# Performance work log

Measured on AMD Instinct MI355X. Metric: run time of the kernel, lower is better.

## Reference

```python
import jax, jax.numpy as jnp
import numpy as np

B, T, D, H, DFF, E = 4, 1024, 1024, 16, 4096, 8
DH = D // H
EPS = 1e-6


def setup_inputs() -> dict:
    key = jax.random.key(0)
    ks = jax.random.split(key, 16)
    s = 0.02
    return {
        "x": jax.random.normal(ks[0], (B, T, D), jnp.float32),
        "mask": jnp.ones((B, 1, 1, T), jnp.bool_),
        "Wq": jax.random.normal(ks[1], (D, D), jnp.float32) * s,
        "bq": jnp.zeros((D,), jnp.float32),
        "Wk": jax.random.normal(ks[2], (D, D), jnp.float32) * s,
        "bk": jnp.zeros((D,), jnp.float32),
        "Wv": jax.random.normal(ks[3], (D, D), jnp.float32) * s,
        "bv": jnp.zeros((D,), jnp.float32),
        "Wo": jax.random.normal(ks[4], (D, D), jnp.float32) * s,
        "bo": jnp.zeros((D,), jnp.float32),
        "ln1_a": jnp.ones((D,), jnp.float32),
        "ln1_b": jnp.zeros((D,), jnp.float32),
        "ln2_a": jnp.ones((D,), jnp.float32),
        "ln2_b": jnp.zeros((D,), jnp.float32),
        "gW": jax.random.normal(ks[5], (D, E), jnp.float32) * s,
        "gb": jnp.zeros((E,), jnp.float32),
        "W1": jax.random.normal(ks[6], (E, D, DFF), jnp.float32) * s,
        "b1": jnp.zeros((E, DFF), jnp.float32),
        "W2": jax.random.normal(ks[7], (E, DFF, D), jnp.float32) * s,
        "b2": jnp.zeros((E, D), jnp.float32),
    }


def layer_norm(x, a, b):
    # Faithful to source: torch std is unbiased (ddof=1), divides by (std + eps)
    mean = jnp.mean(x, -1, keepdims=True)
    std = jnp.std(x, -1, keepdims=True, ddof=1)
    return a * (x - mean) / (std + EPS) + b


def mha(x, mask, Wq, bq, Wk, bk, Wv, bv, Wo, bo):
    def split(h):
        return h.reshape(B, T, H, DH).transpose(0, 2, 1, 3)  # [B,H,T,DH]
    q = split(x @ Wq + bq)
    k = split(x @ Wk + bk)
    v = split(x @ Wv + bv)
    scores = jnp.einsum("bhqd,bhkd->bhqk", q, k) / jnp.sqrt(jnp.float32(DH))
    scores = jnp.where(mask, scores, jnp.float32(-1e9))
    attn = jax.nn.softmax(scores, axis=-1)
    out = jnp.einsum("bhqk,bhkd->bhqd", attn, v)
    out = out.transpose(0, 2, 1, 3).reshape(B, T, D)
    return out @ Wo + bo


def moe(xf, gW, gb, W1, b1, W2, b2):
    # xf: [N, D] flat tokens; top-1 Switch routing
    gate_probs = jax.nn.softmax(xf @ gW + gb, axis=-1)  # [N, E]
    top1_idx = jnp.argmax(gate_probs, axis=-1)          # [N]
    top1_p = jnp.max(gate_probs, axis=-1)               # [N]
    out = jnp.zeros_like(xf)
    for e in range(E):  # fixed small structural loop over experts
        h = jax.nn.relu(xf @ W1[e] + b1[e])
        oe = h @ W2[e] + b2[e]
        sel = (top1_idx == e).astype(xf.dtype)
        out = out + (sel * top1_p)[:, None] * oe
    counts = jax.nn.one_hot(top1_idx, E, dtype=jnp.float32).sum(0)
    aux_loss = jnp.sum((counts / (B * T)) ** 2) * E
    return out, aux_loss


def reference(x, mask, Wq, bq, Wk, bk, Wv, bv, Wo, bo,
              ln1_a, ln1_b, ln2_a, ln2_b, gW, gb, W1, b1, W2, b2):
    # sublayer[0]: x + attn(norm(x))  (dropout=0, inference)
    x1 = x + mha(layer_norm(x, ln1_a, ln1_b), mask, Wq, bq, Wk, bk, Wv, bv, Wo, bo)
    # MoE applied to x1 directly (source calls feed_forward(x), not on the norm)
    ff_out, aux_loss = moe(x1.reshape(-1, D), gW, gb, W1, b1, W2, b2)
    # sublayer[1] with lambda _: ff_out  -> x1 + ff_out (norm computed but discarded)
    x2 = x1 + ff_out.reshape(B, T, D)
    return x2, aux_loss
```

## Files before the change

kernel.cpp:

```cpp
#include <hip/hip_runtime.h>

#define DEV __device__ __forceinline__

typedef unsigned short u16;
typedef __bf16 bf16x8 __attribute__((ext_vector_type(8)));
typedef float f32x4 __attribute__((ext_vector_type(4)));
typedef unsigned short us8 __attribute__((ext_vector_type(8)));

static constexpr int Bn = 4, Tn = 1024, Dn = 1024, Hn = 16, DFFn = 4096, En = 8;
static constexpr int Nn = Bn * Tn;
static constexpr int MAXT64 = 72;
static constexpr int MAXT = 40;
static constexpr int HROWS = 5120;

static constexpr int MT64_E = 0, MT64_P0 = 72;
static constexpr int MT_E = 144, MT_P0 = 184;
static constexpr int MCNT = 224, MCUR = 232, MSEG = 240, MPERM = 248;

static constexpr size_t WQKVT_O = 0;
static constexpr size_t WOT_O   = WQKVT_O + 3ull * 1024 * 1024 * 2;
static constexpr size_t W12T_O  = WOT_O + 1ull * 1024 * 1024 * 2;
static constexpr size_t X1F_O   = W12T_O + 8ull * 1024 * 4096 * 2;
static constexpr size_t XN_O    = X1F_O + (size_t)Nn * Dn * 4;
static constexpr size_t Q_O     = XN_O + (size_t)Nn * Dn * 2;
static constexpr size_t K_O     = Q_O + (size_t)Nn * Dn * 2;
static constexpr size_t VT_O    = K_O + (size_t)Nn * Dn * 2;
static constexpr size_t X1B_O   = VT_O + (size_t)Nn * Dn * 2;
static constexpr size_t P3_O    = XN_O;
static constexpr size_t H_O     = X1B_O + (size_t)Nn * Dn * 2;
static constexpr size_t TOPP_O  = H_O + (size_t)HROWS * DFFn * 2;
static constexpr size_t TIDX_O  = TOPP_O + (size_t)Nn * 4;
static constexpr size_t META_O  = TIDX_O + (size_t)Nn * 4;

DEV u16 f2bf(float f) {
  union { float f; unsigned u; } v; v.f = f;
  unsigned r = v.u + 0x7fffu + ((v.u >> 16) & 1u);
  return (u16)(r >> 16);
}
DEV float bf2f(u16 x) {
  union { unsigned u; float f; } v; v.u = ((unsigned)x) << 16;
  return v.f;
}

DEV void gload16(const void* g, void* l) {
  __builtin_amdgcn_global_load_lds(
      (__attribute__((address_space(1))) void*)(void*)g,
      (__attribute__((address_space(3))) void*)l, 16, 0, 0);
}

DEV void sdecode64(int o, int& row, int& c) {
  row = o >> 7;
  c = ((o >> 4) & 7) ^ (row & 7);
}

DEV int aswz(int r, int c) { return c ^ (r & 7) ^ (((r >> 3) & 3) << 1); }

__global__ __launch_bounds__(256) void tcast4_kernel(
    const float* __restrict__ s0, const float* __restrict__ s1,
    const float* __restrict__ s2, const float* __restrict__ s3,
    u16* __restrict__ wqkvt, u16* __restrict__ wot) {
  __shared__ u16 tile[64][65];
  int z = blockIdx.z;
  const float* src = (z == 0) ? s0 : (z == 1) ? s1 : (z == 2) ? s2 : s3;
  u16* dst = (z < 3) ? wqkvt + (size_t)z * 1024 * 1024 : wot;
  int r0 = blockIdx.y * 64, c0 = blockIdx.x * 64;
  int tr = threadIdx.x >> 4;
  int tc = (threadIdx.x & 15) * 4;
#pragma unroll
  for (int i = 0; i < 4; i++) {
    int r = tr + i * 16;
    float4 v = *reinterpret_cast<const float4*>(&src[(long)(r0 + r) * 1024 + c0 + tc]);
    tile[r][tc + 0] = f2bf(v.x); tile[r][tc + 1] = f2bf(v.y);
    tile[r][tc + 2] = f2bf(v.z); tile[r][tc + 3] = f2bf(v.w);
  }
  __syncthreads();
#pragma unroll
  for (int i = 0; i < 4; i++) {
    int r = tr + i * 16;
    ushort4 o;
    o.x = tile[tc + 0][r]; o.y = tile[tc + 1][r];
    o.z = tile[tc + 2][r]; o.w = tile[tc + 3][r];
    *reinterpret_cast<ushort4*>(&dst[(long)(c0 + r) * 1024 + r0 + tc]) = o;
  }
}

__global__ __launch_bounds__(256) void tcast_kernel(
    const float* __restrict__ src, u16* __restrict__ dst,
    int R, int C, long srcBatch, long dstBatch) {
  __shared__ u16 tile[64][65];
  src += (long)blockIdx.z * srcBatch;
  dst += (long)blockIdx.z * dstBatch;
  int r0 = blockIdx.y * 64, c0 = blockIdx.x * 64;
  int tr = threadIdx.x >> 4;
  int tc = (threadIdx.x & 15) * 4;
#pragma unroll
  for (int i = 0; i < 4; i++) {
    int r = tr + i * 16;
    float4 v = *reinterpret_cast<const float4*>(&src[(long)(r0 + r) * C + c0 + tc]);
    tile[r][tc + 0] = f2bf(v.x); tile[r][tc + 1] = f2bf(v.y);
    tile[r][tc + 2] = f2bf(v.z); tile[r][tc + 3] = f2bf(v.w);
  }
  __syncthreads();
#pragma unroll
  for (int i = 0; i < 4; i++) {
    int r = tr + i * 16;
    ushort4 o;
    o.x = tile[tc + 0][r]; o.y = tile[tc + 1][r];
    o.z = tile[tc + 2][r]; o.w = tile[tc + 3][r];
    *reinterpret_cast<ushort4*>(&dst[(long)(c0 + r) * R + r0 + tc]) = o;
  }
}

__global__ __launch_bounds__(256) void ln_kernel(
    const float* __restrict__ x, const float* __restrict__ a,
    const float* __restrict__ b, u16* __restrict__ xn) {
  __shared__ float red[8];
  int row = blockIdx.x, tid = threadIdx.x;
  int lane = tid & 63, w = tid >> 6;
  float4 v = *reinterpret_cast<const float4*>(&x[(size_t)row * 1024 + tid * 4]);
  float s = v.x + v.y + v.z + v.w;
  float sq = v.x * v.x + v.y * v.y + v.z * v.z + v.w * v.w;
#pragma unroll
  for (int sh = 1; sh <= 32; sh <<= 1) { s += __shfl_xor(s, sh); sq += __shfl_xor(sq, sh); }
  if (lane == 0) { red[w] = s; red[4 + w] = sq; }
  __syncthreads();
  s = red[0] + red[1] + red[2] + red[3];
  sq = red[4] + red[5] + red[6] + red[7];
  float mean = s * (1.0f / 1024.0f);
  float var = (sq - s * mean) * (1.0f / 1023.0f);
  float inv = 1.0f / (sqrtf(var) + 1e-6f);
  float4 av = *reinterpret_cast<const float4*>(&a[tid * 4]);
  float4 bv = *reinterpret_cast<const float4*>(&b[tid * 4]);
  ushort4 o;
  o.x = f2bf(av.x * (v.x - mean) * inv + bv.x);
  o.y = f2bf(av.y * (v.y - mean) * inv + bv.y);
  o.z = f2bf(av.z * (v.z - mean) * inv + bv.z);
  o.w = f2bf(av.w * (v.w - mean) * inv + bv.w);
  *reinterpret_cast<ushort4*>(&xn[(size_t)row * 1024 + tid * 4]) = o;
}

template <int MODE, int NG, int KSPLIT>
__global__ __launch_bounds__(256, 6) void gemm3_k(
    const u16* __restrict__ Ag, const u16* __restrict__ Bg,
    const float* __restrict__ f0, const float* __restrict__ f1,
    const float* __restrict__ f2, const float* __restrict__ xres,
    float* __restrict__ x1f, u16* __restrict__ ob0, u16* __restrict__ ob1,
    u16* __restrict__ ob2, u16* __restrict__ pout, const int* __restrict__ meta) {
  constexpr int K = (MODE == 3) ? 4096 : 1024;
  constexpr int KS = K / KSPLIT;
  constexpr int NSUB = KS >> 6;
  constexpr int MT = (MODE <= 1) ? 64 : MAXT64;
  constexpr int NT = (MODE == 0) ? 24 : (MODE == 2) ? 32 : 8;
  constexpr int WR = 32;
  constexpr int MI = 2;
  constexpr int CA = 2;

  __shared__ u16 As[64 * 64];
  __shared__ u16 Bs[128 * 64];

  const int tid = threadIdx.x, lane = tid & 63, w = tid >> 6;
  const int wm = w >> 1, wn = w & 1;
  const int cL = lane >> 4, rl15 = lane & 15;

  constexpr int NWG = MT * NT * KSPLIT;
  constexpr int q8 = NWG >> 3;
  int b = blockIdx.x;
  int lg = (b & 7) * q8 + (b >> 3);
  constexpr int PERG = KSPLIT * MT * NG;
  int g = lg / PERG, rem = lg - g * PERG;
  int s = rem / (MT * NG); rem -= s * (MT * NG);
  int mt = rem / NG;
  int nt = g * NG + (rem - (rem / NG) * NG);

  int m0 = mt * 64, n0 = nt * 128;
  const int k0 = s * KS;
  const u16* Abase = Ag;
  const u16* Bbase = Bg;
  int e = 0, cnt = 0, seg = 0, pos0 = 0;
  if (MODE >= 2) {
    e = meta[MT64_E + mt];
    if (e < 0) return;
    cnt = meta[MCNT + e];
    seg = meta[MSEG + e];
    pos0 = meta[MT64_P0 + mt];
    Bbase = Bg + (size_t)e * 4096 * 1024;
    if (MODE == 3) Abase = Ag + (size_t)(seg + pos0) * 4096;
    m0 = 0;
  }

  const u16* gA[CA];
  const u16* gB[4];
#pragma unroll
  for (int j = 0; j < CA; j++) {
    int row, c;
    sdecode64(j * 4096 + tid * 16, row, c);
    if constexpr (MODE == 2) {
      int pos = pos0 + row; if (pos >= cnt) pos = cnt - 1;
      int tok = meta[MPERM + seg + pos];
      gA[j] = Ag + (size_t)tok * 1024 + k0 + c * 8;
    } else {
      gA[j] = Abase + (size_t)(m0 + row) * K + k0 + c * 8;
    }
  }
#pragma unroll
  for (int j = 0; j < 4; j++) {
    int row, c;
    sdecode64(j * 4096 + tid * 16, row, c);
    gB[j] = Bbase + (size_t)(n0 + row) * K + k0 + c * 8;
  }

  auto STAGE = [&](int t) {
#pragma unroll
    for (int j = 0; j < CA; j++)
      gload16(gA[j] + t * 64, &As[j * 2048 + tid * 8]);
#pragma unroll
    for (int j = 0; j < 4; j++)
      gload16(gB[j] + t * 64, &Bs[j * 2048 + tid * 8]);
  };

  f32x4 acc[MI][4] = {};
  const char* Ab = reinterpret_cast<const char*>(&As[0]);
  const char* Bb = reinterpret_cast<const char*>(&Bs[0]);

  STAGE(0);
  for (int t = 0; t < NSUB; t++) {
    asm volatile("s_waitcnt vmcnt(0)" ::: "memory");
    __builtin_amdgcn_s_barrier();
#pragma unroll
    for (int ph = 0; ph < 2; ph++) {
      bf16x8 af[MI], bfr[4];
#pragma unroll
      for (int mi = 0; mi < MI; mi++) {
        int row = wm * WR + mi * 16 + rl15;
        af[mi] = *reinterpret_cast<const bf16x8*>(
            Ab + row * 128 + ((ph * 64 + cL * 16) ^ ((row & 7) << 4)));
      }
#pragma unroll
      for (int ni = 0; ni < 4; ni++) {
        int row = wn * 64 + ni * 16 + rl15;
        bfr[ni] = *reinterpret_cast<const bf16x8*>(
            Bb + row * 128 + ((ph * 64 + cL * 16) ^ ((row & 7) << 4)));
      }
#pragma unroll
      for (int mi = 0; mi < MI; mi++)
#pragma unroll
        for (int ni = 0; ni < 4; ni++)
          acc[mi][ni] = __builtin_amdgcn_mfma_f32_16x16x32_bf16(
              af[mi], bfr[ni], acc[mi][ni], 0, 0, 0);
    }
    __builtin_amdgcn_s_barrier();
    if (t + 1 < NSUB) STAGE(t + 1);
  }

  const int cl = rl15, rl = cL;
  if (MODE == 0) {
    int third = n0 >> 10;
    const float* bias = (third == 0) ? f0 : (third == 1) ? f1 : f2;
    const float qs = (third == 0) ? 0.125f : 1.0f;
#pragma unroll
    for (int ni = 0; ni < 4; ni++) {
      int col = n0 + wn * 64 + ni * 16 + cl;
      int jj = col & 1023;
      float bb_ = bias[jj];
      int hh = jj >> 6, dd = jj & 63;
#pragma unroll
      for (int mi = 0; mi < MI; mi++) {
        int t0 = m0 + wm * WR + mi * 16 + rl * 4;
        int b_ = t0 >> 10, tt = t0 & 1023;
        size_t bh = (size_t)(b_ * Hn + hh);
        if (third == 2) {
          ushort4 o4;
          o4.x = f2bf(acc[mi][ni][0] + bb_); o4.y = f2bf(acc[mi][ni][1] + bb_);
          o4.z = f2bf(acc[mi][ni][2] + bb_); o4.w = f2bf(acc[mi][ni][3] + bb_);
          *reinterpret_cast<ushort4*>(&ob2[(bh * 64 + dd) * 1024 + tt]) = o4;
        } else {
          u16* dst = (third == 0) ? ob0 : ob1;
#pragma unroll
          for (int r = 0; r < 4; r++)
            dst[(bh * 1024 + tt + r) * 64 + dd] = f2bf((acc[mi][ni][r] + bb_) * qs);
        }
      }
    }
  } else if (MODE == 1) {
#pragma unroll
    for (int ni = 0; ni < 4; ni++) {
      int col = n0 + wn * 64 + ni * 16 + cl;
      float bo_ = f0[col];
#pragma unroll
      for (int mi = 0; mi < MI; mi++) {
        int row = m0 + wm * WR + mi * 16 + rl * 4;
#pragma unroll
        for (int r = 0; r < 4; r++) {
          size_t idx = (size_t)(row + r) * 1024 + col;
          float v = acc[mi][ni][r] + bo_ + xres[idx];
          x1f[idx] = v;
          ob0[idx] = f2bf(v);
        }
      }
    }
  } else if (MODE == 2) {
#pragma unroll
    for (int ni = 0; ni < 4; ni++) {
      int col = n0 + wn * 64 + ni * 16 + cl;
      float b1_ = f0[(size_t)e * 4096 + col];
#pragma unroll
      for (int mi = 0; mi < MI; mi++) {
        int pos = pos0 + wm * WR + mi * 16 + rl * 4;
#pragma unroll
        for (int r = 0; r < 4; r++) {
          float v = acc[mi][ni][r] + b1_;
          v = v > 0.0f ? v : 0.0f;
          ob0[(size_t)(seg + pos + r) * 4096 + col] = f2bf(v);
        }
      }
    }
  } else {
#pragma unroll
    for (int ni = 0; ni < 4; ni++) {
      int col = n0 + wn * 64 + ni * 16 + cl;
#pragma unroll
      for (int mi = 0; mi < MI; mi++) {
        int pos = pos0 + wm * WR + mi * 16 + rl * 4;
#pragma unroll
        for (int r = 0; r < 4; r++)
          pout[((size_t)s * HROWS + seg + pos + r) * 1024 + col] = f2bf(acc[mi][ni][r]);
      }
    }
  }
}

__global__ __launch_bounds__(256) void reduce3_kernel(
    const u16* __restrict__ P3, const float* __restrict__ x1f,
    const float* __restrict__ topp, const float* __restrict__ b2,
    const int* __restrict__ meta, float* __restrict__ out) {
  int bidx = blockIdx.x;
  int tile = bidx >> 7, rowin = bidx & 127;
  int e = meta[MT_E + tile];
  if (e < 0) return;
  int cnt = meta[MCNT + e], seg = meta[MSEG + e];
  int pos = meta[MT_P0 + tile] + rowin;
  if (pos >= cnt) return;
  int tok = meta[MPERM + seg + pos];
  size_t prow = (size_t)(seg + pos) * 1024;
  float p = topp[tok];
  int c = threadIdx.x * 4;
  ushort4 u0 = *reinterpret_cast<const ushort4*>(&P3[prow + c]);
  ushort4 u1 = *reinterpret_cast<const ushort4*>(&P3[(size_t)HROWS * 1024 + prow + c]);
  float4 xr = *reinterpret_cast<const float4*>(&x1f[(size_t)tok * 1024 + c]);
  float4 bb = *reinterpret_cast<const float4*>(&b2[e * 1024 + c]);
  float4 o;
  o.x = xr.x + p * (bf2f(u0.x) + bf2f(u1.x) + bb.x);
  o.y = xr.y + p * (bf2f(u0.y) + bf2f(u1.y) + bb.y);
  o.z = xr.z + p * (bf2f(u0.z) + bf2f(u1.z) + bb.z);
  o.w = xr.w + p * (bf2f(u0.w) + bf2f(u1.w) + bb.w);
  *reinterpret_cast<float4*>(&out[(size_t)tok * 1024 + c]) = o;
}

__global__ __launch_bounds__(256, 4) void attn_kernel(
    const u16* __restrict__ q, const u16* __restrict__ k,
    const u16* __restrict__ vt, u16* __restrict__ attn) {
  __shared__ u16 Ks[2][64 * 64];
  __shared__ u16 Vs[2][64 * 64];
  const int tid = threadIdx.x, lane = tid & 63, w = tid >> 6;
  const int g = lane >> 4, l15 = lane & 15;

  int bb = blockIdx.x;
  int lg = (bb & 7) * 128 + (bb >> 3);
  const int bh = lg >> 4;
  const int qt = lg & 15;
  const size_t qkbase = (size_t)bh * Tn * 64;
  const size_t vtbase = (size_t)bh * 64 * Tn;
  const int qrow0 = qt * 64 + w * 16;

  bf16x8 qf[2];
  {
    const u16* qp = q + qkbase + (size_t)(qrow0 + l15) * 64 + g * 8;
    qf[0] = *reinterpret_cast<const bf16x8*>(qp);
    qf[1] = *reinterpret_cast<const bf16x8*>(qp + 32);
  }

  const u16* gk[2];
  const u16* gv[2];
#pragma unroll
  for (int j = 0; j < 2; j++) {
    int sidx = j * 256 + tid;
    int r = sidx >> 3, p = sidx & 7;
    int c = aswz(r, p);
    gk[j] = k + qkbase + (size_t)r * 64 + c * 8;
    gv[j] = vt + vtbase + (size_t)r * Tn + c * 8;
  }

  auto STAGE = [&](int t) {
    int buf = t & 1;
#pragma unroll
    for (int j = 0; j < 2; j++) {
      int sidx = j * 256 + tid;
      gload16(gk[j] + (size_t)t * 4096, &Ks[buf][sidx * 8]);
      gload16(gv[j] + (size_t)t * 64, &Vs[buf][sidx * 8]);
    }
  };

  f32x4 o[4] = {};
  float mrun = -1e30f, lsum = 0.0f;

  STAGE(0);
  for (int t = 0; t < 16; t++) {
    asm volatile("s_waitcnt vmcnt(0)" ::: "memory");
    __builtin_amdgcn_s_barrier();
    if (t + 1 < 16) STAGE(t + 1);

    const char* Kb = reinterpret_cast<const char*>(&Ks[t & 1][0]);
    const char* Vb = reinterpret_cast<const char*>(&Vs[t & 1][0]);

    f32x4 sk[2][2];
#pragma unroll
    for (int kb = 0; kb < 2; kb++)
#pragma unroll
      for (int m = 0; m < 2; m++) {
        f32x4 sa = {};
#pragma unroll
        for (int ph = 0; ph < 2; ph++) {
          int ksel = kb * 32 + (l15 >> 2) * 8 + m * 4 + (lane & 3);
          int pch = aswz(ksel, g + ph * 4);
          bf16x8 kf = *reinterpret_cast<const bf16x8*>(Kb + ksel * 128 + pch * 16);
          sa = __builtin_amdgcn_mfma_f32_16x16x32_bf16(kf, qf[ph], sa, 0, 0, 0);
        }
        sk[kb][m] = sa;
      }

    float mx = -1e30f;
#pragma unroll
    for (int kb = 0; kb < 2; kb++)
#pragma unroll
      for (int m = 0; m < 2; m++)
#pragma unroll
        for (int r = 0; r < 4; r++) mx = fmaxf(mx, sk[kb][m][r]);
    mx = fmaxf(mx, __shfl_xor(mx, 16));
    mx = fmaxf(mx, __shfl_xor(mx, 32));
    float mn = fmaxf(mrun, mx);
    float rsc = __expf(mrun - mn);
    mrun = mn;

    float pv[2][8];
    float ps = 0.0f;
#pragma unroll
    for (int kb = 0; kb < 2; kb++)
#pragma unroll
      for (int m = 0; m < 2; m++)
#pragma unroll
        for (int r = 0; r < 4; r++) {
          float pe = __expf(sk[kb][m][r] - mn);
          pv[kb][m * 4 + r] = pe;
          ps += pe;
        }
    ps += __shfl_xor(ps, 16);
    ps += __shfl_xor(ps, 32);
    lsum = lsum * rsc + ps;
#pragma unroll
    for (int nf = 0; nf < 4; nf++)
#pragma unroll
      for (int r = 0; r < 4; r++) o[nf][r] *= rsc;

    bf16x8 pf[2];
#pragma unroll
    for (int kb = 0; kb < 2; kb++)
#pragma unroll
      for (int j = 0; j < 8; j++) pf[kb][j] = (__bf16)pv[kb][j];

#pragma unroll
    for (int nf = 0; nf < 4; nf++) {
      int d = nf * 16 + l15;
#pragma unroll
      for (int kb = 0; kb < 2; kb++) {
        int pch = aswz(d, g + kb * 4);
        bf16x8 vf = *reinterpret_cast<const bf16x8*>(Vb + d * 128 + pch * 16);
        o[nf] = __builtin_amdgcn_mfma_f32_16x16x32_bf16(vf, pf[kb], o[nf], 0, 0, 0);
      }
    }
  }

  __syncthreads();
  u16* T = &Ks[0][0];
  float inv = 1.0f / lsum;
#pragma unroll
  for (int nf = 0; nf < 4; nf++)
#pragma unroll
    for (int r = 0; r < 4; r++) {
      int row = w * 16 + l15;
      int d = nf * 16 + g * 4 + r;
      int off = (row << 6) + ((((d >> 3) ^ (row & 7)) << 3) | (d & 7));
      T[off] = f2bf(o[nf][r] * inv);
    }
  __syncthreads();
  int b_ = bh >> 4, h_ = bh & 15;
#pragma unroll
  for (int p = 0; p < 2; p++) {
    int idx = p * 256 + tid;
    int row = idx >> 3, ch = idx & 7;
    int pch = ch ^ (row & 7);
    us8 v = *reinterpret_cast<const us8*>(T + (row << 6) + (pch << 3));
    *reinterpret_cast<us8*>(
        &attn[((size_t)(b_ * Tn + qt * 64 + row)) * 1024 + h_ * 64 + ch * 8]) = v;
  }
}

__global__ __launch_bounds__(256) void gate_kernel(
    const float* __restrict__ x1f, const float* __restrict__ gW,
    const float* __restrict__ gb, float* __restrict__ topp,
    int* __restrict__ tidx, int* __restrict__ meta) {
  int lane = threadIdx.x & 63;
  int n = blockIdx.x * 4 + (threadIdx.x >> 6);
  float acc[8] = {};
  const float* xr = x1f + (size_t)n * 1024;
  for (int kk = 0; kk < 16; kk++) {
    int kcol = kk * 64 + lane;
    float xv = xr[kcol];
    float4 g0 = *reinterpret_cast<const float4*>(&gW[kcol * 8]);
    float4 g1 = *reinterpret_cast<const float4*>(&gW[kcol * 8 + 4]);
    acc[0] = fmaf(xv, g0.x, acc[0]); acc[1] = fmaf(xv, g0.y, acc[1]);
    acc[2] = fmaf(xv, g0.z, acc[2]); acc[3] = fmaf(xv, g0.w, acc[3]);
    acc[4] = fmaf(xv, g1.x, acc[4]); acc[5] = fmaf(xv, g1.y, acc[5]);
    acc[6] = fmaf(xv, g1.z, acc[6]); acc[7] = fmaf(xv, g1.w, acc[7]);
  }
#pragma unroll
  for (int e2 = 0; e2 < 8; e2++)
#pragma unroll
    for (int sh = 1; sh <= 32; sh <<= 1) acc[e2] += __shfl_xor(acc[e2], sh);
  if (lane == 0) {
    float best = -1e30f; int bi = 0;
#pragma unroll
    for (int e2 = 0; e2 < 8; e2++) {
      float lgt = acc[e2] + gb[e2];
      if (lgt > best) { best = lgt; bi = e2; }
    }
    float den = 0.0f;
#pragma unroll
    for (int e2 = 0; e2 < 8; e2++) den += __expf(acc[e2] + gb[e2] - best);
    topp[n] = 1.0f / den;
    tidx[n] = bi;
    atomicAdd(&meta[MCNT + bi], 1);
  }
}

__global__ void scan_kernel(int* meta, float* aux_out) {
  if (threadIdx.x == 0) {
    int sb = 0, t64 = 0, t1 = 0;
    float aux = 0.0f;
    for (int e2 = 0; e2 < 8; e2++) {
      meta[MSEG + e2] = sb;
      int c = meta[MCNT + e2];
      int n64 = (c + 63) >> 6;
      for (int i = 0; i < n64; i++) { meta[MT64_E + t64] = e2; meta[MT64_P0 + t64] = i * 64; t64++; }
      int n1 = (c + 127) >> 7;
      for (int i = 0; i < n1; i++) { meta[MT_E + t1] = e2; meta[MT_P0 + t1] = i * 128; t1++; }
      sb += n1 << 7;
      float fr = (float)c * (1.0f / 4096.0f);
      aux += fr * fr;
    }
    for (; t64 < MAXT64; t64++) { meta[MT64_E + t64] = -1; meta[MT64_P0 + t64] = 0; }
    for (; t1 < MAXT; t1++) { meta[MT_E + t1] = -1; meta[MT_P0 + t1] = 0; }
    aux_out[0] = aux * 8.0f;
  }
}

__global__ __launch_bounds__(256) void scatter_kernel(const int* __restrict__ tidx, int* meta) {
  int n = blockIdx.x * 256 + threadIdx.x;
  int e2 = tidx[n];
  int pos = atomicAdd(&meta[MCUR + e2], 1);
  meta[MPERM + meta[MSEG + e2] + pos] = n;
}

extern "C" void kernel_launch(void* const* d_in, const int* in_sizes, int n_in,
                              void* d_out, int out_size, void* d_ws, size_t ws_size,
                              hipStream_t stream) {
  const float* x   = (const float*)d_in[0];
  const float* Wq  = (const float*)d_in[2];
  const float* bq  = (const float*)d_in[3];
  const float* Wk  = (const float*)d_in[4];
  const float* bk  = (const float*)d_in[5];
  const float* Wv  = (const float*)d_in[6];
  const float* bv  = (const float*)d_in[7];
  const float* Wo  = (const float*)d_in[8];
  const float* bo  = (const float*)d_in[9];
  const float* ln1a = (const float*)d_in[10];
  const float* ln1b = (const float*)d_in[11];
  const float* gW  = (const float*)d_in[14];
  const float* gb  = (const float*)d_in[15];
  const float* W1  = (const float*)d_in[16];
  const float* b1  = (const float*)d_in[17];
  const float* W2  = (const float*)d_in[18];
  const float* b2  = (const float*)d_in[19];
  float* out = (float*)d_out;
  char* ws = (char*)d_ws;

  u16* wqkvt = (u16*)(ws + WQKVT_O);
  u16* wot   = (u16*)(ws + WOT_O);
  u16* w12t  = (u16*)(ws + W12T_O);
  u16* xn    = (u16*)(ws + XN_O);
  u16* qb    = (u16*)(ws + Q_O);
  u16* kb    = (u16*)(ws + K_O);
  u16* vtb   = (u16*)(ws + VT_O);
  float* x1f = (float*)(ws + X1F_O);
  u16* x1b   = (u16*)(ws + X1B_O);
  u16* p3    = (u16*)(ws + P3_O);
  u16* hb    = (u16*)(ws + H_O);
  float* topp = (float*)(ws + TOPP_O);
  int* tidx  = (int*)(ws + TIDX_O);
  int* meta  = (int*)(ws + META_O);

  hipMemsetAsync(meta + MCNT, 0, 16 * sizeof(int), stream);

  tcast4_kernel<<<dim3(16, 16, 4), 256, 0, stream>>>(Wq, Wk, Wv, Wo, wqkvt, wot);
  tcast_kernel<<<dim3(64, 16, 8), 256, 0, stream>>>(W1, w12t, 1024, 4096,
                                                    (long)1024 * 4096, (long)4096 * 1024);

  ln_kernel<<<4096, 256, 0, stream>>>(x, ln1a, ln1b, xn);
  gemm3_k<0, 4, 1><<<1536, 256, 0, stream>>>(xn, wqkvt, bq, bk, bv, nullptr, nullptr,
                                             qb, kb, vtb, nullptr, meta);
  attn_kernel<<<1024, 256, 0, stream>>>(qb, kb, vtb, xn);
  gemm3_k<1, 4, 1><<<512, 256, 0, stream>>>(xn, wot, bo, nullptr, nullptr, x, x1f,
                                            x1b, nullptr, nullptr, nullptr, meta);
  gate_kernel<<<1024, 256, 0, stream>>>(x1f, gW, gb, topp, tidx, meta);
  scan_kernel<<<1, 64, 0, stream>>>(meta, out + (size_t)Nn * Dn);
  scatter_kernel<<<16, 256, 0, stream>>>(tidx, meta);
  gemm3_k<2, 4, 1><<<2304, 256, 0, stream>>>(x1b, w12t, b1, nullptr, nullptr, nullptr,
                                             nullptr, hb, nullptr, nullptr, nullptr, meta);
  tcast_kernel<<<dim3(16, 64, 8), 256, 0, stream>>>(W2, w12t, 4096, 1024,
                                                    (long)4096 * 1024, (long)1024 * 4096);
  gemm3_k<3, 2, 2><<<1152, 256, 0, stream>>>(hb, w12t, nullptr, nullptr, nullptr, nullptr,
                                             nullptr, nullptr, nullptr, nullptr, p3, meta);
  reduce3_kernel<<<MAXT * 128, 256, 0, stream>>>(p3, x1f, topp, b2, meta, out);
}
```

Measured before the change: 399.5 us.

## Add double-buffered GEMM kernel for QKV/FFN1 and use 128-row tiles for FFN2

Adds a new gemm5_k kernel that double-buffers the A and B shared-memory tiles and uses explicit vmcnt waits, so the global-to-LDS load of the next K-slice overlaps MFMA work on the current one. The QKV projection and expert FFN1 GEMMs now use it. The remaining gemm3_k is parameterised by BM, and the FFN2 GEMM switches to 128-row tiles (using the MT_E/MT_P0 tile metadata), which cuts its grid from 1152 to 640 blocks and raises B-tile reuse. In exchange, LDS per block doubles, launch bounds drop to 3 blocks per CU, and register pressure goes up, so occupancy falls.

```diff
diff --git a/kernel.cpp b/kernel.cpp
--- a/kernel.cpp
+++ b/kernel.cpp
@@ -46,6 +46,11 @@
   __builtin_amdgcn_global_load_lds(
       (__attribute__((address_space(1))) void*)(void*)g,
       (__attribute__((address_space(3))) void*)l, 16, 0, 0);
+}
+
+template <int N> DEV void waitvm() {
+  if constexpr (N == 0) asm volatile("s_waitcnt vmcnt(0)" ::: "memory");
+  else if constexpr (N == 6) asm volatile("s_waitcnt vmcnt(6)" ::: "memory");
 }
 
 DEV void sdecode64(int o, int& row, int& c) {
@@ -139,23 +144,178 @@
   *reinterpret_cast<ushort4*>(&xn[(size_t)row * 1024 + tid * 4]) = o;
 }
 
-template <int MODE, int NG, int KSPLIT>
-__global__ __launch_bounds__(256, 6) void gemm3_k(
+template <int MODE, int NG>
+__global__ __launch_bounds__(256, 3) void gemm5_k(
     const u16* __restrict__ Ag, const u16* __restrict__ Bg,
     const float* __restrict__ f0, const float* __restrict__ f1,
-    const float* __restrict__ f2, const float* __restrict__ xres,
-    float* __restrict__ x1f, u16* __restrict__ ob0, u16* __restrict__ ob1,
-    u16* __restrict__ ob2, u16* __restrict__ pout, const int* __restrict__ meta) {
+    const float* __restrict__ f2, u16* __restrict__ ob0, u16* __restrict__ ob1,
+    u16* __restrict__ ob2, const int* __restrict__ meta) {
+  constexpr int NSUB = 16;
+  constexpr int MT = (MODE == 0) ? 64 : MAXT64;
+  constexpr int NT = (MODE == 0) ? 24 : 32;
+  constexpr int MI = 2;
+
+  __shared__ u16 As[2][64 * 64];
+  __shared__ u16 Bs[2][128 * 64];
+
+  const int tid = threadIdx.x, lane = tid & 63, w = tid >> 6;
+  const int wm = w >> 1, wn = w & 1;
+  const int cL = lane >> 4, rl15 = lane & 15;
+
+  constexpr int NWG = MT * NT;
+  constexpr int q8 = NWG >> 3;
+  int b = blockIdx.x;
+  int lg = (b & 7) * q8 + (b >> 3);
+  constexpr int PERG = MT * NG;
+  int g = lg / PERG, rem = lg - g * PERG;
+  int mt = rem / NG;
+  int nt = g * NG + (rem - (rem / NG) * NG);
+
+  int m0 = mt * 64, n0 = nt * 128;
+  const u16* Bbase = Bg;
+  int e = 0, cnt = 0, seg = 0, pos0 = 0;
+  if constexpr (MODE == 2) {
+    e = meta[MT64_E + mt];
+    if (e < 0) return;
+    cnt = meta[MCNT + e];
+    seg = meta[MSEG + e];
+    pos0 = meta[MT64_P0 + mt];
+    Bbase = Bg + (size_t)e * 4096 * 1024;
+  }
+
+  const u16* gA[2];
+  const u16* gB[4];
+#pragma unroll
+  for (int j = 0; j < 2; j++) {
+    int row, c;
+    sdecode64(j * 4096 + tid * 16, row, c);
+    if constexpr (MODE == 2) {
+      int pos = pos0 + row; if (pos >= cnt) pos = cnt - 1;
+      int tok = meta[MPERM + seg + pos];
+      gA[j] = Ag + (size_t)tok * 1024 + c * 8;
+    } else {
+      gA[j] = Ag + (size_t)(m0 + row) * 1024 + c * 8;
+    }
+  }
+#pragma unroll
+  for (int j = 0; j < 4; j++) {
+    int row, c;
+    sdecode64(j * 4096 + tid * 16, row, c);
+    gB[j] = Bbase + (size_t)(n0 + row) * 1024 + c * 8;
+  }
+
+  auto STAGE = [&](int t) {
+    int bi = t & 1;
+#pragma unroll
+    for (int j = 0; j < 2; j++)
+      gload16(gA[j] + t * 64, &As[bi][j * 2048 + tid * 8]);
+#pragma unroll
+    for (int j = 0; j < 4; j++)
+      gload16(gB[j] + t * 64, &Bs[bi][j * 2048 + tid * 8]);
+  };
+
+  f32x4 acc[MI][4] = {};
+
+  STAGE(0);
+  for (int t = 0; t < NSUB; t++) {
+    if (t + 1 < NSUB) {
+      STAGE(t + 1);
+      waitvm<6>();
+    } else {
+      waitvm<0>();
+    }
+    __builtin_amdgcn_s_barrier();
+    const char* Ab = reinterpret_cast<const char*>(&As[t & 1][0]);
+    const char* Bb = reinterpret_cast<const char*>(&Bs[t & 1][0]);
+#pragma unroll
+    for (int ph = 0; ph < 2; ph++) {
+      bf16x8 af[MI], bfr[4];
+#pragma unroll
+      for (int mi = 0; mi < MI; mi++) {
+        int row = wm * 32 + mi * 16 + rl15;
+        af[mi] = *reinterpret_cast<const bf16x8*>(
+            Ab + row * 128 + ((ph * 64 + cL * 16) ^ ((row & 7) << 4)));
+      }
+#pragma unroll
+      for (int ni = 0; ni < 4; ni++) {
+        int row = wn * 64 + ni * 16 + rl15;
+        bfr[ni] = *reinterpret_cast<const bf16x8*>(
+            Bb + row * 128 + ((ph * 64 + cL * 16) ^ ((row & 7) << 4)));
+      }
+#pragma unroll
+      for (int mi = 0; mi < MI; mi++)
+#pragma unroll
+        for (int ni = 0; ni < 4; ni++)
+          acc[mi][ni] = __builtin_amdgcn_mfma_f32_16x16x32_bf16(
+              af[mi], bfr[ni], acc[mi][ni], 0, 0, 0);
+    }
+    __builtin_amdgcn_s_barrier();
+  }
+
+  const int cl = rl15, rl = cL;
+  if constexpr (MODE == 0) {
+    int third = n0 >> 10;
+    const float* bias = (third == 0) ? f0 : (third == 1) ? f1 : f2;
+    const float qs = (third == 0) ? 0.125f : 1.0f;
+#pragma unroll
+    for (int ni = 0; ni < 4; ni++) {
+      int col = n0 + wn * 64 + ni * 16 + cl;
+      int jj = col & 1023;
+      float bb_ = bias[jj];
+      int hh = jj >> 6, dd = jj & 63;
+#pragma unroll
+      for (int mi = 0; mi < MI; mi++) {
+        int t0 = m0 + wm * 32 + mi * 16 + rl * 4;
+        int b_ = t0 >> 10, tt = t0 & 1023;
+        size_t bh = (size_t)(b_ * Hn + hh);
+        if (third == 2) {
+          ushort4 o4;
+          o4.x = f2bf(acc[mi][ni][0] + bb_); o4.y = f2bf(acc[mi][ni][1] + bb_);
+          o4.z = f2bf(acc[mi][ni][2] + bb_); o4.w = f2bf(acc[mi][ni][3] + bb_);
+          *reinterpret_cast<ushort4*>(&ob2[(bh * 64 + dd) * 1024 + tt]) = o4;
+        } else {
+          u16* dst = (third == 0) ? ob0 : ob1;
+#pragma unroll
+          for (int r = 0; r < 4; r++)
+            dst[(bh * 1024 + tt + r) * 64 + dd] = f2bf((acc[mi][ni][r] + bb_) * qs);
+        }
+      }
+    }
+  } else {
+#pragma unroll
+    for (int ni = 0; ni < 4; ni++) {
+      int col = n0 + wn * 64 + ni * 16 + cl;
+      float b1_ = f0[(size_t)e * 4096 + col];
+#pragma unroll
+      for (int mi = 0; mi < MI; mi++) {
+        int pos = pos0 + wm * 32 + mi * 16 + rl * 4;
+#pragma unroll
+        for (int r = 0; r < 4; r++) {
+          float v = acc[mi][ni][r] + b1_;
+          v = v > 0.0f ? v : 0.0f;
+          ob0[(size_t)(seg + pos + r) * 4096 + col] = f2bf(v);
+        }
+      }
+    }
+  }
+}
+
+template <int MODE, int BM, int NG, int KSPLIT>
+__global__ __launch_bounds__(256, 3) void gemm3_k(
+    const u16* __restrict__ Ag, const u16* __restrict__ Bg,
+    const float* __restrict__ f0, const float* __restrict__ xres,
+    float* __restrict__ x1f, u16* __restrict__ ob0,
+    u16* __restrict__ pout, const int* __restrict__ meta) {
   constexpr int K = (MODE == 3) ? 4096 : 1024;
   constexpr int KS = K / KSPLIT;
   constexpr int NSUB = KS >> 6;
-  constexpr int MT = (MODE <= 1) ? 64 : MAXT64;
-  constexpr int NT = (MODE == 0) ? 24 : (MODE == 2) ? 32 : 8;
-  constexpr int WR = 32;
-  constexpr int MI = 2;
-  constexpr int CA = 2;
-
-  __shared__ u16 As[64 * 64];
+  constexpr int MT = (MODE == 1) ? (4096 / BM) : MAXT;
+  constexpr int NT = 8;
+  constexpr int WR = BM / 2;
+  constexpr int MI = WR / 16;
+  constexpr int CA = BM / 32;
+
+  __shared__ u16 As[BM * 64];
   __shared__ u16 Bs[128 * 64];
 
   const int tid = threadIdx.x, lane = tid & 63, w = tid >> 6;
@@ -172,19 +332,18 @@
   int mt = rem / NG;
   int nt = g * NG + (rem - (rem / NG) * NG);
 
-  int m0 = mt * 64, n0 = nt * 128;
+  int m0 = mt * BM, n0 = nt * 128;
   const int k0 = s * KS;
   const u16* Abase = Ag;
   const u16* Bbase = Bg;
-  int e = 0, cnt = 0, seg = 0, pos0 = 0;
-  if (MODE >= 2) {
-    e = meta[MT64_E + mt];
+  int e = 0, seg = 0, pos0 = 0;
+  if constexpr (MODE == 3) {
+    e = meta[MT_E + mt];
     if (e < 0) return;
-    cnt = meta[MCNT + e];
     seg = meta[MSEG + e];
-    pos0 = meta[MT64_P0 + mt];
+    pos0 = meta[MT_P0 + mt];
     Bbase = Bg + (size_t)e * 4096 * 1024;
-    if (MODE == 3) Abase = Ag + (size_t)(seg + pos0) * 4096;
+    Abase = Ag + (size_t)(seg + pos0) * 4096;
     m0 = 0;
   }
 
@@ -194,13 +353,7 @@
   for (int j = 0; j < CA; j++) {
     int row, c;
     sdecode64(j * 4096 + tid * 16, row, c);
-    if constexpr (MODE == 2) {
-      int pos = pos0 + row; if (pos >= cnt) pos = cnt - 1;
-      int tok = meta[MPERM + seg + pos];
-      gA[j] = Ag + (size_t)tok * 1024 + k0 + c * 8;
-    } else {
-      gA[j] = Abase + (size_t)(m0 + row) * K + k0 + c * 8;
-    }
+    gA[j] = Abase + (size_t)(m0 + row) * K + k0 + c * 8;
   }
 #pragma unroll
   for (int j = 0; j < 4; j++) {
@@ -253,35 +406,7 @@
   }
 
   const int cl = rl15, rl = cL;
-  if (MODE == 0) {
-    int third = n0 >> 10;
-    const float* bias = (third == 0) ? f0 : (third == 1) ? f1 : f2;
-    const float qs = (third == 0) ? 0.125f : 1.0f;
-#pragma unroll
-    for (int ni = 0; ni < 4; ni++) {
-      int col = n0 + wn * 64 + ni * 16 + cl;
-      int jj = col & 1023;
-      float bb_ = bias[jj];
-      int hh = jj >> 6, dd = jj & 63;
-#pragma unroll
-      for (int mi = 0; mi < MI; mi++) {
-        int t0 = m0 + wm * WR + mi * 16 + rl * 4;
-        int b_ = t0 >> 10, tt = t0 & 1023;
-        size_t bh = (size_t)(b_ * Hn + hh);
-        if (third == 2) {
-          ushort4 o4;
-          o4.x = f2bf(acc[mi][ni][0] + bb_); o4.y = f2bf(acc[mi][ni][1] + bb_);
-          o4.z = f2bf(acc[mi][ni][2] + bb_); o4.w = f2bf(acc[mi][ni][3] + bb_);
-          *reinterpret_cast<ushort4*>(&ob2[(bh * 64 + dd) * 1024 + tt]) = o4;
-        } else {
-          u16* dst = (third == 0) ? ob0 : ob1;
-#pragma unroll
-          for (int r = 0; r < 4; r++)
-            dst[(bh * 1024 + tt + r) * 64 + dd] = f2bf((acc[mi][ni][r] + bb_) * qs);
-        }
-      }
-    }
-  } else if (MODE == 1) {
+  if constexpr (MODE == 1) {
 #pragma unroll
     for (int ni = 0; ni < 4; ni++) {
       int col = n0 + wn * 64 + ni * 16 + cl;
@@ -295,22 +420,6 @@
           float v = acc[mi][ni][r] + bo_ + xres[idx];
           x1f[idx] = v;
           ob0[idx] = f2bf(v);
-        }
-      }
-    }
-  } else if (MODE == 2) {
-#pragma unroll
-    for (int ni = 0; ni < 4; ni++) {
-      int col = n0 + wn * 64 + ni * 16 + cl;
-      float b1_ = f0[(size_t)e * 4096 + col];
-#pragma unroll
-      for (int mi = 0; mi < MI; mi++) {
-        int pos = pos0 + wm * WR + mi * 16 + rl * 4;
-#pragma unroll
-        for (int r = 0; r < 4; r++) {
-          float v = acc[mi][ni][r] + b1_;
-          v = v > 0.0f ? v : 0.0f;
-          ob0[(size_t)(seg + pos + r) * 4096 + col] = f2bf(v);
         }
       }
     }
@@ -615,19 +724,17 @@
                                                     (long)1024 * 4096, (long)4096 * 1024);
 
   ln_kernel<<<4096, 256, 0, stream>>>(x, ln1a, ln1b, xn);
-  gemm3_k<0, 4, 1><<<1536, 256, 0, stream>>>(xn, wqkvt, bq, bk, bv, nullptr, nullptr,
-                                             qb, kb, vtb, nullptr, meta);
+  gemm5_k<0, 4><<<1536, 256, 0, stream>>>(xn, wqkvt, bq, bk, bv, qb, kb, vtb, meta);
   attn_kernel<<<1024, 256, 0, stream>>>(qb, kb, vtb, xn);
-  gemm3_k<1, 4, 1><<<512, 256, 0, stream>>>(xn, wot, bo, nullptr, nullptr, x, x1f,
-                                            x1b, nullptr, nullptr, nullptr, meta);
+  gemm3_k<1, 64, 4, 1><<<512, 256, 0, stream>>>(xn, wot, bo, x, x1f, x1b, nullptr, meta);
   gate_kernel<<<1024, 256, 0, stream>>>(x1f, gW, gb, topp, tidx, meta);
   scan_kernel<<<1, 64, 0, stream>>>(meta, out + (size_t)Nn * Dn);
   scatter_kernel<<<16, 256, 0, stream>>>(tidx, meta);
-  gemm3_k<2, 4, 1><<<2304, 256, 0, stream>>>(x1b, w12t, b1, nullptr, nullptr, nullptr,
-                                             nullptr, hb, nullptr, nullptr, nullptr, meta);
+  gemm5_k<2, 4><<<2304, 256, 0, stream>>>(x1b, w12t, b1, nullptr, nullptr, hb, nullptr,
+                                          nullptr, meta);
   tcast_kernel<<<dim3(16, 64, 8), 256, 0, stream>>>(W2, w12t, 4096, 1024,
                                                     (long)4096 * 1024, (long)1024 * 4096);
-  gemm3_k<3, 2, 2><<<1152, 256, 0, stream>>>(hb, w12t, nullptr, nullptr, nullptr, nullptr,
-                                             nullptr, nullptr, nullptr, nullptr, p3, meta);
+  gemm3_k<3, 128, 2, 2><<<640, 256, 0, stream>>>(hb, w12t, nullptr, nullptr, nullptr,
+                                                 nullptr, p3, meta);
   reduce3_kernel<<<MAXT * 128, 256, 0, stream>>>(p3, x1f, topp, b2, meta, out);
 }
```

After: 380.0 us. 4.9% less time.
